# Kernel tuning notes

Measured on AMD Instinct MI355X. Metric: run time of the kernel, lower is better.

## Reference

```python
import jax, jax.numpy as jnp
import numpy as np

DEPTH = 9
NUM_LEAVES = 2 ** DEPTH            # 512
NUM_BRANCHES = 2 ** DEPTH - 1      # 511


def _leaf_paths(depth):
    """For each leaf, the BFS (heap-order) branch indices along its root->leaf
    path and the left/right bit taken at each branch (1 = right)."""
    L = 2 ** depth
    idx = np.zeros((L, depth), np.int32)
    bits = np.zeros((L, depth), np.int32)
    for l in range(L):
        node = 0
        for t in range(depth):
            b = (l >> (depth - 1 - t)) & 1
            idx[l, t] = node
            bits[l, t] = b
            node = 2 * node + 1 + b
    return jnp.asarray(idx), jnp.asarray(bits)

PATH_IDX, PATH_BITS = _leaf_paths(DEPTH)


def setup_inputs() -> dict:
    key = jax.random.key(0)
    k1, k2, k3 = jax.random.split(key, 3)
    B, D, W, H = 128, 256, 28, 28
    C = 200
    return {
        "xs": jax.random.normal(k1, (B, D, W, H), jnp.float32),
        "prototypes": jax.random.normal(k2, (NUM_BRANCHES, D, 1, 1), jnp.float32),
        "leaf_params": jax.random.normal(k3, (NUM_LEAVES, C), jnp.float32),
    }


def reference(xs, prototypes, leaf_params):
    # ---- L2Conv2D: squared-L2 distance map via conv decomposition ----
    B, D, W, H = xs.shape
    P = prototypes.shape[0]
    p = prototypes.reshape(P, D)                       # W1 = H1 = 1
    x2 = jnp.sum(xs * xs, axis=1)                      # [B, W, H]
    p2 = jnp.sum(p * p, axis=1)                        # [P]
    xp = jnp.einsum('bdwh,pd->bpwh', xs, p)            # [B, P, W, H]
    sq = x2[:, None] - 2.0 * xp + p2[None, :, None, None]
    distances = jnp.sqrt(jnp.abs(sq) + 1e-14)          # [B, P, W, H]

    # ---- min-pool over full spatial extent (avg-pool unused: focal off) ----
    min_distances = jnp.min(distances, axis=(2, 3))    # [B, P]
    similarities = jnp.exp(-min_distances)             # [B, P], ps per branch

    # ---- soft tree routing: pa(leaf) = prod over path of ps / (1-ps) ----
    ps_path = similarities[:, PATH_IDX]                # [B, L, depth]
    step = jnp.where(PATH_BITS[None] == 1, ps_path, 1.0 - ps_path)
    pa = jnp.prod(step, axis=-1)                       # [B, L]

    # ---- mix leaf class distributions (distributed sampling strategy) ----
    ds = jax.nn.softmax(leaf_params, axis=-1)          # [L, C]
    return pa @ ds                                     # [B, C]
```

## Files before the change

kernel.cpp:

```cpp
#include <hip/hip_runtime.h>
#include <hip/hip_bf16.h>

typedef __attribute__((ext_vector_type(8))) int   i32x8;
typedef __attribute__((ext_vector_type(4))) int   i32x4;
typedef __attribute__((ext_vector_type(4))) float f32x4;

#define D_K    256
#define WH     784
#define WHH    392
#define P_REAL 511
#define P_PAD  512
#define C_OUT  200
#define NLEAF  512
#define TDEPTH 9

#define NT      32
#define NTILES  13
#define TILE_B  8192

#define WS_PB8  0
#define WS_P2   131072
#define WS_DS   133120
#define WS_PM   542720

#define SCALE_ONE 0x7F7F7F7F

__global__ __launch_bounds__(64)
void prep2_kernel(const float* __restrict__ protos, const float* __restrict__ lp,
                  unsigned char* __restrict__ pb8, float* __restrict__ p2,
                  float* __restrict__ ds) {
    int bid = blockIdx.x;
    int l = threadIdx.x;
    if (bid < P_PAD) {
        int p = bid;
        f32x4 v = {0.f, 0.f, 0.f, 0.f};
        if (p < P_REAL)
            v = *reinterpret_cast<const f32x4*>(protos + (size_t)p * D_K + 4 * l);
        int u = 0;
        u = __builtin_amdgcn_cvt_pk_fp8_f32(-2.f * v[0], -2.f * v[1], u, false);
        u = __builtin_amdgcn_cvt_pk_fp8_f32(-2.f * v[2], -2.f * v[3], u, true);
        *reinterpret_cast<int*>(pb8 + (size_t)p * D_K + 4 * l) = u;
        float s = v[0]*v[0] + v[1]*v[1] + v[2]*v[2] + v[3]*v[3];
#pragma unroll
        for (int m = 32; m >= 1; m >>= 1) s += __shfl_xor(s, m, 64);
        if (l == 0) p2[p] = s;
    } else {
        int row = bid - P_PAD;
        float v[4];
        float mx = -3.4e38f;
#pragma unroll
        for (int i = 0; i < 4; ++i) {
            int c = l + 64 * i;
            v[i] = (c < C_OUT) ? lp[(size_t)row * C_OUT + c] : -3.4e38f;
            mx = fmaxf(mx, v[i]);
        }
#pragma unroll
        for (int m = 32; m >= 1; m >>= 1) mx = fmaxf(mx, __shfl_xor(mx, m, 64));
        float sum = 0.f;
#pragma unroll
        for (int i = 0; i < 4; ++i) {
            int c = l + 64 * i;
            if (c < C_OUT) { v[i] = expf(v[i] - mx); sum += v[i]; }
        }
#pragma unroll
        for (int m = 32; m >= 1; m >>= 1) sum += __shfl_xor(sum, m, 64);
        float inv = 1.f / sum;
#pragma unroll
        for (int i = 0; i < 4; ++i) {
            int c = l + 64 * i;
            if (c < C_OUT) ds[(size_t)row * C_OUT + c] = v[i] * inv;
        }
    }
}

__global__ __launch_bounds__(512, 2)
void proto_min_kernel(const float* __restrict__ xs,
                      const unsigned char* __restrict__ pb8,
                      float* __restrict__ pm) {
    __shared__ unsigned char Xs[2][TILE_B];
    __shared__ float x2buf[2][8*68 + 8];

    const int tid  = threadIdx.x;
    const int wv   = tid >> 6;
    const int lane = tid & 63;
    const int lh   = lane >> 4;
    const int lr   = lane & 15;

    const int b   = blockIdx.x >> 1;
    const int whh = blockIdx.x & 1;

    const float* xb = xs + (size_t)b * (D_K * WH) + whh * WHH;

    i32x8 af[4][2];
#pragma unroll
    for (int mf = 0; mf < 4; ++mf) {
        const unsigned char* rp = pb8 + (size_t)(64*wv + 16*mf + lr) * D_K + lh*32;
        af[mf][0] = *reinterpret_cast<const i32x8*>(rp);
        af[mf][1] = *reinterpret_cast<const i32x8*>(rp + 128);
    }

    const int n4 = tid & 7;
    const int kq = tid >> 3;

    f32x4 rmin[4];
#pragma unroll
    for (int mf = 0; mf < 4; ++mf)
        rmin[mf] = (f32x4){3.0e38f, 3.0e38f, 3.0e38f, 3.0e38f};

    f32x4 ld[4];

#define LOAD_TILE(T) do {                                                     \
        int colb = (T) * NT + 4 * n4;                                         \
        if (colb > WHH - 4) colb = WHH - 4;                                   \
        const float* rowp = xb + (size_t)(4*kq) * WH + colb;                  \
        _Pragma("unroll")                                                     \
        for (int r = 0; r < 4; ++r)                                           \
            ld[r] = *reinterpret_cast<const f32x4*>(rowp + r * WH);           \
    } while (0)

#define STAGE_TILE(DST) do {                                                  \
        f32x4 x2a = {0.f, 0.f, 0.f, 0.f};                                     \
        _Pragma("unroll")                                                     \
        for (int r = 0; r < 4; ++r) {                                         \
            f32x4 v = ld[r];                                                  \
            x2a[0] += v[0]*v[0]; x2a[1] += v[1]*v[1];                         \
            x2a[2] += v[2]*v[2]; x2a[3] += v[3]*v[3];                         \
        }                                                                     \
        _Pragma("unroll")                                                     \
        for (int c = 0; c < 4; ++c) {                                         \
            int n = 4*n4 + c;                                                 \
            int key = (n ^ (n >> 2)) & 7;                                     \
            int u = 0;                                                        \
            u = __builtin_amdgcn_cvt_pk_fp8_f32(ld[0][c], ld[1][c], u, false);\
            u = __builtin_amdgcn_cvt_pk_fp8_f32(ld[2][c], ld[3][c], u, true); \
            int off = n*256 + (((kq >> 2) ^ key) << 4) + ((kq & 3) << 2);     \
            *reinterpret_cast<int*>(&Xs[DST][off]) = u;                       \
        }                                                                     \
        _Pragma("unroll")                                                     \
        for (int c = 0; c < 4; ++c) {                                         \
            x2a[c] += __shfl_xor(x2a[c], 8, 64);                              \
            x2a[c] += __shfl_xor(x2a[c], 16, 64);                             \
            x2a[c] += __shfl_xor(x2a[c], 32, 64);                             \
        }                                                                     \
        if (lane < 8) {                                                       \
            _Pragma("unroll")                                                 \
            for (int c = 0; c < 4; ++c)                                       \
                x2buf[DST][lane*68 + c*8 + wv] = x2a[c];                      \
        }                                                                     \
    } while (0)

    LOAD_TILE(0);
    STAGE_TILE(0);
    __syncthreads();

    int buf = 0;
    for (int t = 0; t < NTILES; ++t) {
        const bool more = (t + 1 < NTILES);

        if (more) LOAD_TILE(t + 1);

        float x2v[2];
#pragma unroll
        for (int nf = 0; nf < 2; ++nf) {
            int n = 16*nf + lr;
            const float* xp = &x2buf[buf][(n >> 2)*68 + (n & 3)*8];
            f32x4 q0 = *reinterpret_cast<const f32x4*>(xp);
            f32x4 q1 = *reinterpret_cast<const f32x4*>(xp + 4);
            x2v[nf] = ((q0[0]+q0[1]) + (q0[2]+q0[3]))
                    + ((q1[0]+q1[1]) + (q1[2]+q1[3]));
        }

        f32x4 acc[4][2];
#pragma unroll
        for (int mf = 0; mf < 4; ++mf) {
            acc[mf][0] = (f32x4){x2v[0], x2v[0], x2v[0], x2v[0]};
            acc[mf][1] = (f32x4){x2v[1], x2v[1], x2v[1], x2v[1]};
        }

        __builtin_amdgcn_s_setprio(1);
#pragma unroll
        for (int ks = 0; ks < 2; ++ks) {
            i32x8 bfr[2];
#pragma unroll
            for (int nf = 0; nf < 2; ++nf) {
                int n = 16*nf + lr;
                int key = (n ^ (n >> 2)) & 7;
                int kg0 = ks*8 + lh*2;
                i32x4 lo = *reinterpret_cast<const i32x4*>(
                               &Xs[buf][n*256 + ((kg0 ^ key) << 4)]);
                i32x4 hi = *reinterpret_cast<const i32x4*>(
                               &Xs[buf][n*256 + (((kg0 + 1) ^ key) << 4)]);
                bfr[nf] = __builtin_shufflevector(lo, hi, 0,1,2,3,4,5,6,7);
            }
#pragma unroll
            for (int mf = 0; mf < 4; ++mf)
#pragma unroll
                for (int nf = 0; nf < 2; ++nf)
                    acc[mf][nf] = __builtin_amdgcn_mfma_scale_f32_16x16x128_f8f6f4(
                        af[mf][ks], bfr[nf], acc[mf][nf],
                        0, 0,
                        0, SCALE_ONE,
                        0, SCALE_ONE);
        }
        __builtin_amdgcn_s_setprio(0);

        if (more) STAGE_TILE(buf ^ 1);

#pragma unroll
        for (int mf = 0; mf < 4; ++mf)
#pragma unroll
            for (int r = 0; r < 4; ++r)
                rmin[mf][r] = fminf(rmin[mf][r],
                                    fminf(acc[mf][0][r], acc[mf][1][r]));

        __syncthreads();
        buf ^= 1;
    }

#pragma unroll
    for (int mf = 0; mf < 4; ++mf)
#pragma unroll
        for (int r = 0; r < 4; ++r) {
            float v = rmin[mf][r];
#pragma unroll
            for (int m = 1; m <= 8; m <<= 1)
                v = fminf(v, __shfl_xor(v, m, 64));
            rmin[mf][r] = v;
        }

    if (lr == 0) {
        float* pmw = pm + ((size_t)b * 2 + whh) * P_PAD;
#pragma unroll
        for (int mf = 0; mf < 4; ++mf)
#pragma unroll
            for (int r = 0; r < 4; ++r)
                pmw[64*wv + 16*mf + 4*lh + r] = rmin[mf][r];
    }
#undef LOAD_TILE
#undef STAGE_TILE
}

__global__ __launch_bounds__(256)
void out_kernel(const float* __restrict__ pm, const float* __restrict__ p2,
                const float* __restrict__ ds, float* __restrict__ out) {
    __shared__ float sim[NLEAF];
    __shared__ float pa[NLEAF];
    int b = blockIdx.x;
    int t = threadIdx.x;
    const float* pm0 = pm + (size_t)b * 2 * P_PAD;
#pragma unroll
    for (int j = 0; j < 2; ++j) {
        int p = t + 256 * j;
        float m = fminf(pm0[p], pm0[P_PAD + p]);
        float sq = m + p2[p];
        sim[p] = expf(-sqrtf(fabsf(sq) + 1e-14f));
    }
    __syncthreads();
#pragma unroll
    for (int j = 0; j < 2; ++j) {
        int leaf = t + 256 * j;
        int node = 0;
        float prod = 1.f;
#pragma unroll
        for (int st = 0; st < TDEPTH; ++st) {
            int bit = (leaf >> (TDEPTH - 1 - st)) & 1;
            float sv = sim[node];
            prod *= bit ? sv : (1.f - sv);
            node = 2 * node + 1 + bit;
        }
        pa[leaf] = prod;
    }
    __syncthreads();
    if (t < C_OUT) {
        float a0 = 0.f, a1 = 0.f, a2 = 0.f, a3 = 0.f;
        for (int l = 0; l < NLEAF; l += 4) {
            a0 += pa[l + 0] * ds[(size_t)(l + 0) * C_OUT + t];
            a1 += pa[l + 1] * ds[(size_t)(l + 1) * C_OUT + t];
            a2 += pa[l + 2] * ds[(size_t)(l + 2) * C_OUT + t];
            a3 += pa[l + 3] * ds[(size_t)(l + 3) * C_OUT + t];
        }
        out[(size_t)b * C_OUT + t] = (a0 + a1) + (a2 + a3);
    }
}

extern "C" void kernel_launch(void* const* d_in, const int* in_sizes, int n_in,
                              void* d_out, int out_size, void* d_ws, size_t ws_size,
                              hipStream_t stream) {
    (void)in_sizes; (void)n_in; (void)out_size; (void)ws_size;
    const float* xs     = (const float*)d_in[0];
    const float* protos = (const float*)d_in[1];
    const float* lp     = (const float*)d_in[2];
    float* out = (float*)d_out;

    char* ws = (char*)d_ws;
    unsigned char* pb8 = (unsigned char*)(ws + WS_PB8);
    float* p2   = (float*)(ws + WS_P2);
    float* dsm  = (float*)(ws + WS_DS);
    float* pm   = (float*)(ws + WS_PM);

    prep2_kernel<<<1024, 64, 0, stream>>>(protos, lp, pb8, p2, dsm);
    proto_min_kernel<<<256, 512, 0, stream>>>(xs, pb8, pm);
    out_kernel<<<128, 256, 0, stream>>>(pm, p2, dsm, out);
}
```

Before: 52.39 us.

## Split prototype dimension across four blocks with XCD-aware block remapping

The proto_min kernel now launches 1024 blocks of 256 threads, each handling 128 prototypes for one (batch, half-spatial) slice instead of all 512. Block IDs are remapped so that the four blocks sharing the same input slice land on the same XCD and can share L2. Each thread loads and stages two K-quarters per tile, with the second load interleaved after the MFMA work. The intent is to fill more CUs, since the old 256-block grid covered each CU only once. In exchange, each xs tile is loaded and converted to fp8 four times rather than once, which adds memory traffic and conversion work.

Result: slower. 90.83 us (+73.4%).

```diff
diff --git a/kernel.cpp b/kernel.cpp
--- a/kernel.cpp
+++ b/kernel.cpp
@@ -73,12 +73,12 @@
     }
 }
 
-__global__ __launch_bounds__(512, 2)
+__global__ __launch_bounds__(256, 4)
 void proto_min_kernel(const float* __restrict__ xs,
                       const unsigned char* __restrict__ pb8,
                       float* __restrict__ pm) {
     __shared__ unsigned char Xs[2][TILE_B];
-    __shared__ float x2buf[2][8*68 + 8];
+    __shared__ float x2buf[2][8][4][4];
 
     const int tid  = threadIdx.x;
     const int wv   = tid >> 6;
@@ -86,40 +86,47 @@
     const int lh   = lane >> 4;
     const int lr   = lane & 15;
 
-    const int b   = blockIdx.x >> 1;
-    const int whh = blockIdx.x & 1;
+    const int id  = blockIdx.x;
+    const int xcd = id & 7;
+    const int t3  = id >> 3;
+    const int q   = t3 & 3;
+    const int grp = ((t3 >> 2) << 3) | xcd;
+    const int b   = grp >> 1;
+    const int whh = grp & 1;
+    const int p0  = q * 128;
 
     const float* xb = xs + (size_t)b * (D_K * WH) + whh * WHH;
 
-    i32x8 af[4][2];
-#pragma unroll
-    for (int mf = 0; mf < 4; ++mf) {
-        const unsigned char* rp = pb8 + (size_t)(64*wv + 16*mf + lr) * D_K + lh*32;
+    i32x8 af[2][2];
+#pragma unroll
+    for (int mf = 0; mf < 2; ++mf) {
+        const unsigned char* rp = pb8 + (size_t)(p0 + 32*wv + 16*mf + lr) * D_K + lh*32;
         af[mf][0] = *reinterpret_cast<const i32x8*>(rp);
         af[mf][1] = *reinterpret_cast<const i32x8*>(rp + 128);
     }
 
-    const int n4 = tid & 7;
-    const int kq = tid >> 3;
-
-    f32x4 rmin[4];
-#pragma unroll
-    for (int mf = 0; mf < 4; ++mf)
+    const int n4  = tid & 7;
+    const int kq0 = tid >> 3;
+
+    f32x4 rmin[2];
+#pragma unroll
+    for (int mf = 0; mf < 2; ++mf)
         rmin[mf] = (f32x4){3.0e38f, 3.0e38f, 3.0e38f, 3.0e38f};
 
     f32x4 ld[4];
-
-#define LOAD_TILE(T) do {                                                     \
+    f32x4 x2a;
+
+#define LOAD_H(T, I) do {                                                     \
         int colb = (T) * NT + 4 * n4;                                         \
         if (colb > WHH - 4) colb = WHH - 4;                                   \
-        const float* rowp = xb + (size_t)(4*kq) * WH + colb;                  \
+        const float* rowp = xb + (size_t)(4*(kq0 + 32*(I))) * WH + colb;      \
         _Pragma("unroll")                                                     \
         for (int r = 0; r < 4; ++r)                                           \
             ld[r] = *reinterpret_cast<const f32x4*>(rowp + r * WH);           \
     } while (0)
 
-#define STAGE_TILE(DST) do {                                                  \
-        f32x4 x2a = {0.f, 0.f, 0.f, 0.f};                                     \
+#define STAGE_H(I, DST) do {                                                  \
+        int kq = kq0 + 32*(I);                                                \
         _Pragma("unroll")                                                     \
         for (int r = 0; r < 4; ++r) {                                         \
             f32x4 v = ld[r];                                                  \
@@ -136,6 +143,9 @@
             int off = n*256 + (((kq >> 2) ^ key) << 4) + ((kq & 3) << 2);     \
             *reinterpret_cast<int*>(&Xs[DST][off]) = u;                       \
         }                                                                     \
+    } while (0)
+
+#define X2_FINISH(DST) do {                                                   \
         _Pragma("unroll")                                                     \
         for (int c = 0; c < 4; ++c) {                                         \
             x2a[c] += __shfl_xor(x2a[c], 8, 64);                              \
@@ -144,35 +154,33 @@
         }                                                                     \
         if (lane < 8) {                                                       \
             _Pragma("unroll")                                                 \
-            for (int c = 0; c < 4; ++c)                                       \
-                x2buf[DST][lane*68 + c*8 + wv] = x2a[c];                      \
+            for (int c = 0; c < 4; ++c) x2buf[DST][lane][c][wv] = x2a[c];     \
         }                                                                     \
     } while (0)
 
-    LOAD_TILE(0);
-    STAGE_TILE(0);
+    x2a = (f32x4){0.f, 0.f, 0.f, 0.f};
+    LOAD_H(0, 0); STAGE_H(0, 0);
+    LOAD_H(0, 1); STAGE_H(1, 0);
+    X2_FINISH(0);
     __syncthreads();
 
     int buf = 0;
     for (int t = 0; t < NTILES; ++t) {
         const bool more = (t + 1 < NTILES);
 
-        if (more) LOAD_TILE(t + 1);
+        if (more) LOAD_H(t + 1, 0);
 
         float x2v[2];
 #pragma unroll
         for (int nf = 0; nf < 2; ++nf) {
             int n = 16*nf + lr;
-            const float* xp = &x2buf[buf][(n >> 2)*68 + (n & 3)*8];
-            f32x4 q0 = *reinterpret_cast<const f32x4*>(xp);
-            f32x4 q1 = *reinterpret_cast<const f32x4*>(xp + 4);
-            x2v[nf] = ((q0[0]+q0[1]) + (q0[2]+q0[3]))
-                    + ((q1[0]+q1[1]) + (q1[2]+q1[3]));
-        }
-
-        f32x4 acc[4][2];
-#pragma unroll
-        for (int mf = 0; mf < 4; ++mf) {
+            f32x4 qv = *reinterpret_cast<const f32x4*>(&x2buf[buf][n >> 2][n & 3][0]);
+            x2v[nf] = (qv[0] + qv[1]) + (qv[2] + qv[3]);
+        }
+
+        f32x4 acc[2][2];
+#pragma unroll
+        for (int mf = 0; mf < 2; ++mf) {
             acc[mf][0] = (f32x4){x2v[0], x2v[0], x2v[0], x2v[0]};
             acc[mf][1] = (f32x4){x2v[1], x2v[1], x2v[1], x2v[1]};
         }
@@ -193,32 +201,39 @@
                 bfr[nf] = __builtin_shufflevector(lo, hi, 0,1,2,3,4,5,6,7);
             }
 #pragma unroll
-            for (int mf = 0; mf < 4; ++mf)
+            for (int mf = 0; mf < 2; ++mf)
 #pragma unroll
                 for (int nf = 0; nf < 2; ++nf)
                     acc[mf][nf] = __builtin_amdgcn_mfma_scale_f32_16x16x128_f8f6f4(
                         af[mf][ks], bfr[nf], acc[mf][nf],
-                        0, 0,
-                        0, SCALE_ONE,
-                        0, SCALE_ONE);
+                        0, 0, 0, SCALE_ONE, 0, SCALE_ONE);
         }
         __builtin_amdgcn_s_setprio(0);
 
-        if (more) STAGE_TILE(buf ^ 1);
-
-#pragma unroll
-        for (int mf = 0; mf < 4; ++mf)
+        if (more) {
+            x2a = (f32x4){0.f, 0.f, 0.f, 0.f};
+            STAGE_H(0, buf ^ 1);
+            LOAD_H(t + 1, 1);
+        }
+
+#pragma unroll
+        for (int mf = 0; mf < 2; ++mf)
 #pragma unroll
             for (int r = 0; r < 4; ++r)
                 rmin[mf][r] = fminf(rmin[mf][r],
                                     fminf(acc[mf][0][r], acc[mf][1][r]));
 
+        if (more) {
+            STAGE_H(1, buf ^ 1);
+            X2_FINISH(buf ^ 1);
+        }
+
         __syncthreads();
         buf ^= 1;
     }
 
 #pragma unroll
-    for (int mf = 0; mf < 4; ++mf)
+    for (int mf = 0; mf < 2; ++mf)
 #pragma unroll
         for (int r = 0; r < 4; ++r) {
             float v = rmin[mf][r];
@@ -231,13 +246,14 @@
     if (lr == 0) {
         float* pmw = pm + ((size_t)b * 2 + whh) * P_PAD;
 #pragma unroll
-        for (int mf = 0; mf < 4; ++mf)
+        for (int mf = 0; mf < 2; ++mf)
 #pragma unroll
             for (int r = 0; r < 4; ++r)
-                pmw[64*wv + 16*mf + 4*lh + r] = rmin[mf][r];
-    }
-#undef LOAD_TILE
-#undef STAGE_TILE
+                pmw[p0 + 32*wv + 16*mf + 4*lh + r] = rmin[mf][r];
+    }
+#undef LOAD_H
+#undef STAGE_H
+#undef X2_FINISH
 }
 
 __global__ __launch_bounds__(256)
@@ -299,6 +315,6 @@
     float* pm   = (float*)(ws + WS_PM);
 
     prep2_kernel<<<1024, 64, 0, stream>>>(protos, lp, pb8, p2, dsm);
-    proto_min_kernel<<<256, 512, 0, stream>>>(xs, pb8, pm);
+    proto_min_kernel<<<1024, 256, 0, stream>>>(xs, pb8, pm);
     out_kernel<<<128, 256, 0, stream>>>(pm, p2, dsm, out);
 }
```
